# Optimization experiments

Measured on AMD Instinct MI355X. Metric: run time of the kernel, lower is better.

The kernel has to match this reference:

```python
import jax, jax.numpy as jnp
from jax import lax
import numpy as np

LRELU_SLOPE = 0.01  # PyTorch LeakyReLU default
BETA = 0.25


def lrelu(x):
    return jnp.where(x >= 0, x, LRELU_SLOPE * x)


def conv2d(x, w, b, stride, pad):
    # x: [B,C,H,W], w: [Cout,Cin,k,k] (torch OIHW)
    y = lax.conv_general_dilated(x, w, (stride, stride), ((pad, pad), (pad, pad)),
                                 dimension_numbers=('NCHW', 'OIHW', 'NCHW'))
    return y + b[None, :, None, None]


def conv_transpose2d(x, w, b, stride, out_pad):
    # w: torch ConvTranspose2d weight [Cin,Cout,k,k]; implement as dilated conv
    # with spatially flipped kernel. out = (i-1)*stride + k + out_pad.
    wf = jnp.flip(w, (2, 3)).transpose(1, 0, 2, 3)  # -> [Cout,Cin,k,k]
    k = w.shape[2]
    pad = ((k - 1, k - 1 + out_pad), (k - 1, k - 1 + out_pad))
    y = lax.conv_general_dilated(x, wf, (1, 1), pad, lhs_dilation=(stride, stride),
                                 dimension_numbers=('NCHW', 'OIHW', 'NCHW'))
    return y + b[None, :, None, None]


def setup_inputs() -> dict:
    key = jax.random.key(0)
    ks = jax.random.split(key, 16)
    s = 0.05
    inp = {
        'x':   jax.random.normal(ks[0], (64, 1, 256, 256), jnp.float32),
        'ew1': jax.random.normal(ks[1], (8, 1, 4, 4), jnp.float32) * s,
        'eb1': jnp.zeros((8,), jnp.float32),
        'ew2': jax.random.normal(ks[2], (16, 8, 4, 4), jnp.float32) * s,
        'eb2': jnp.zeros((16,), jnp.float32),
        'ew3': jax.random.normal(ks[3], (32, 16, 4, 4), jnp.float32) * s,
        'eb3': jnp.zeros((32,), jnp.float32),
        'ew4': jax.random.normal(ks[4], (32, 32, 3, 3), jnp.float32) * s,
        'eb4': jnp.zeros((32,), jnp.float32),
        'ew5': jax.random.normal(ks[5], (64, 32, 1, 1), jnp.float32) * s,
        'eb5': jnp.zeros((64,), jnp.float32),
        'dw1': jax.random.normal(ks[6], (32, 64, 3, 3), jnp.float32) * s,
        'db1': jnp.zeros((32,), jnp.float32),
        'dw2': jax.random.normal(ks[7], (32, 16, 4, 4), jnp.float32) * s,
        'db2': jnp.zeros((16,), jnp.float32),
        'dw3': jax.random.normal(ks[8], (16, 8, 4, 4), jnp.float32) * s,
        'db3': jnp.zeros((8,), jnp.float32),
        'dw4': jax.random.normal(ks[9], (8, 1, 4, 4), jnp.float32) * s,
        'db4': jnp.zeros((1,), jnp.float32),
        # nn.init.uniform_(-1/K, 1/K) with K=512
        'codebook': jax.random.uniform(ks[10], (512, 64), jnp.float32,
                                       minval=-1.0 / 512, maxval=1.0 / 512),
    }
    return inp


def vqvae_forward(x, ew1, eb1, ew2, eb2, ew3, eb3, ew4, eb4, ew5, eb5,
                  dw1, db1, dw2, db2, dw3, db3, dw4, db4, codebook):
    # ---- encoder ----
    h = lrelu(conv2d(x, ew1, eb1, 2, 0))   # [B,8,127,127]
    h = lrelu(conv2d(h, ew2, eb2, 2, 0))   # [B,16,62,62]
    h = lrelu(conv2d(h, ew3, eb3, 2, 0))   # [B,32,30,30]
    h = lrelu(conv2d(h, ew4, eb4, 1, 1))   # [B,32,30,30]
    h = lrelu(conv2d(h, ew5, eb5, 1, 0))   # [B,64,30,30]
    # ---- vector quantizer ----
    lat = h.transpose(0, 2, 3, 1)                      # [B,h,w,D]
    D = lat.shape[-1]
    flat = lat.reshape(-1, D)                          # [N,D]
    # squared euclidean distances via expansion (same argmin as torch.norm)
    d2 = (jnp.sum(flat * flat, axis=1, keepdims=True)
          - 2.0 * flat @ codebook.T
          + jnp.sum(codebook * codebook, axis=1))      # [N,K]
    idx = jnp.argmin(d2, axis=1)                       # [N]
    q = codebook[idx].reshape(lat.shape)               # [B,h,w,D]
    commitment = jnp.mean((lax.stop_gradient(q) - lat) ** 2)
    embedding = jnp.mean((q - lax.stop_gradient(lat)) ** 2)
    vq_loss = commitment * BETA + embedding
    q_st = lat + lax.stop_gradient(q - lat)            # straight-through
    z = q_st.transpose(0, 3, 1, 2)                     # [B,D,h,w]
    # ---- decoder ----
    h = lrelu(conv2d(z, dw1, db1, 1, 1))               # [B,32,30,30]
    h = lrelu(conv_transpose2d(h, dw2, db2, 2, 1))     # [B,16,63,63]
    h = lrelu(conv_transpose2d(h, dw3, db3, 2, 1))     # [B,8,131,131]
    recons = jnp.tanh(conv_transpose2d(h, dw4, db4, 2, 0))  # [B,1,264,264]
    return recons, vq_loss


def reference(x, ew1, eb1, ew2, eb2, ew3, eb3, ew4, eb4, ew5, eb5,
              dw1, db1, dw2, db2, dw3, db3, dw4, db4, codebook):
    return vqvae_forward(x, ew1, eb1, ew2, eb2, ew3, eb3, ew4, eb4, ew5, eb5,
                         dw1, db1, dw2, db2, dw3, db3, dw4, db4, codebook)
```

## Files before the change

### kernel.cpp

```cpp
#include <hip/hip_runtime.h>
#include <hip/hip_bf16.h>
#include <math.h>

#define LRELU 0.01f

template<int NW>
__device__ __forceinline__ void ldw(const float* p, float* w) {
    if constexpr (NW % 4 == 0) {
#pragma unroll
        for (int u = 0; u < NW / 4; u++) {
            float4 v = *(const float4*)(p + 4 * u);
            w[4*u] = v.x; w[4*u+1] = v.y; w[4*u+2] = v.z; w[4*u+3] = v.w;
        }
    } else {
#pragma unroll
        for (int c = 0; c < NW; c++) w[c] = p[c];
    }
}

__device__ __forceinline__ void wfwd(const float* s, float* d, int CIN, int COUT,
                                     int KK, int i) {
    int co = i / (CIN * KK); int r = i - co * CIN * KK;
    int ci = r / KK; int t = r - ci * KK;
    d[(ci * KK + t) * COUT + co] = s[i];
}
__device__ __forceinline__ void wtr(const float* s, float* d, int CIN, int COUT,
                                    int KK, int i) {
    int ci = i / (COUT * KK); int r = i - ci * COUT * KK;
    int co = r / KK; int t = r - co * KK;
    d[(t * CIN + ci) * COUT + co] = s[i];
}
__global__ __launch_bounds__(256)
void prep_k(const float* e1, const float* e2, const float* e3, const float* e4,
            const float* e5, const float* d1, const float* d2, const float* d3,
            const float* d4, float* w, const float* cbp, float* hcbn,
            unsigned long long* keys, float* loss, int* idxm, int N) {
    int i = blockIdx.x * 256 + threadIdx.x;
    if      (i < 128)   wfwd(e1, w + 0,     1,  8, 16, i);
    else if (i < 2176)  wfwd(e2, w + 128,   8, 16, 16, i - 128);
    else if (i < 10368) wfwd(e3, w + 2176, 16, 32, 16, i - 2176);
    else if (i < 19584) wfwd(e4, w + 10368, 32, 32, 9, i - 10368);
    else if (i < 21632) wfwd(e5, w + 19584, 32, 64, 1, i - 19584);
    else if (i < 40064) wfwd(d1, w + 21632, 64, 32, 9, i - 21632);
    else if (i < 48256) wtr (d2, w + 40064, 32, 16, 16, i - 40064);
    else if (i < 50304) wtr (d3, w + 48256, 16,  8, 16, i - 48256);
    else if (i < 50432) wtr (d4, w + 50304,  8,  1, 16, i - 50304);
    else if (i < 50944) {
        int k = i - 50432;
        const float* c = cbp + k * 64;
        float s = 0.f;
#pragma unroll
        for (int d = 0; d < 64; d++) s = fmaf(c[d], c[d], s);
        hcbn[k] = 0.5f * s;
    } else if (i < 50944 + N) {
        keys[i - 50944] = 0xFFFFFFFFFFFFFFFFull;
    } else if (i == 50944 + N) {
        loss[0] = 0.f;
    } else if (i < 50945 + N + 64 * 124) {
        int j = i - (50945 + N);
        int b2 = j / 124, s = j - b2 * 124;
        int r, c;
        if (s < 32)      { r = 0;  c = s; }
        else if (s < 64) { r = 31; c = s - 32; }
        else { int u = s - 64; r = 1 + (u >> 1); c = (u & 1) * 31; }
        idxm[b2 * 1024 + r * 32 + c] = 512;
    }
}

__global__ __launch_bounds__(256)
void ubuild_k(const float* __restrict__ w, const float* __restrict__ cb,
              float* __restrict__ U) {
    int g = blockIdx.x * 256 + threadIdx.x;
    if (g >= 513 * 288) return;
    if (g >= 512 * 288) { U[g] = 0.f; return; }
    int k = g / 288, rem = g - k * 288;
    const float* cr = cb + k * 64;
    float s = 0.f;
#pragma unroll 4
    for (int ci = 0; ci < 64; ci++)
        s = fmaf(w[ci * 288 + rem], cr[ci], s);
    U[g] = s;
}

template<int CIN, int COUT, int CO_BLK, int HIN, int ISTR, int HOUT, int WOUT,
         int OPLANE, int OSTR, int OPAD, int CB, int RB, int ZCONV, int ZF_CH>
__global__ __launch_bounds__(256)
void convs2_k(const float* __restrict__ in, const float* __restrict__ wt,
              const float* __restrict__ bias, float* __restrict__ out) {
    const int b = blockIdx.x, cog = blockIdx.y, tid = threadIdx.x;
    if (ZF_CH > 0 && (int)blockIdx.z >= ZCONV) {
        if (cog != 0) return;
        int i = ((int)blockIdx.z - ZCONV) * 256 + tid;
        if (i >= ZF_CH * 124) return;
        int ch = i / 124, s = i - ch * 124;
        int r, c;
        if (s < 32)      { r = 0;  c = s; }
        else if (s < 64) { r = 31; c = s - 32; }
        else { int u = s - 64; r = 1 + (u >> 1); c = (u & 1) * 31; }
        out[(size_t)(b * ZF_CH + ch) * 1024 + r * 32 + c] = 0.f;
        return;
    }
    __shared__ __align__(16) float lw[CIN * 16 * CO_BLK];
    for (int i = tid; i < CIN * 16 * CO_BLK; i += 256) {
        int row = i / CO_BLK, c = i - row * CO_BLK;
        lw[i] = wt[row * COUT + cog * CO_BLK + c];
    }
    __syncthreads();

    const int tz = blockIdx.z;
    const int cbi = tz / RB, rb = tz - cbi * RB;
    const int tx = tid & 15, ty = tid >> 4;
    const int ow0 = (cbi * 16 + tx) * 2;
    const int oh  = rb * 16 + ty;
    if (oh >= HOUT || ow0 >= WOUT) return;
    const bool p1v = (ow0 + 1) < WOUT;

    float acc[CO_BLK][2];
#pragma unroll
    for (int c = 0; c < CO_BLK; c++) {
        float bv = bias[cog * CO_BLK + c];
        acc[c][0] = bv; acc[c][1] = bv;
    }
    const float* inb = in + ((size_t)(b * CIN) * HIN + oh * 2) * ISTR + ow0 * 2;
#pragma unroll 2
    for (int ci = 0; ci < CIN; ci++) {
        const float* r = inb + (size_t)ci * HIN * ISTR;
        float4 a4[4]; float2 b2[4];
#pragma unroll
        for (int kh = 0; kh < 4; kh++) {
            a4[kh] = *(const float4*)(r + kh * ISTR);
            b2[kh] = p1v ? *(const float2*)(r + kh * ISTR + 4) : make_float2(0.f, 0.f);
        }
        const float* wr = lw + ci * 16 * CO_BLK;
#pragma unroll
        for (int kh = 0; kh < 4; kh++) {
            float x0[4] = {a4[kh].x, a4[kh].y, a4[kh].z, a4[kh].w};
            float x1[4] = {a4[kh].z, a4[kh].w, b2[kh].x, b2[kh].y};
#pragma unroll
            for (int kw = 0; kw < 4; kw++) {
                float wv[CO_BLK];
                ldw<CO_BLK>(wr + (kh * 4 + kw) * CO_BLK, wv);
#pragma unroll
                for (int c = 0; c < CO_BLK; c++) {
                    acc[c][0] = fmaf(x0[kw], wv[c], acc[c][0]);
                    acc[c][1] = fmaf(x1[kw], wv[c], acc[c][1]);
                }
            }
        }
    }
    float* ob = out + (size_t)(b * COUT + cog * CO_BLK) * OPLANE
                    + (oh + OPAD) * OSTR + ow0 + OPAD;
#pragma unroll
    for (int c = 0; c < CO_BLK; c++) {
        float v0 = acc[c][0]; v0 = (v0 >= 0.f) ? v0 : LRELU * v0;
        ob[(size_t)c * OPLANE] = v0;
        if (p1v) {
            float v1 = acc[c][1]; v1 = (v1 >= 0.f) ? v1 : LRELU * v1;
            ob[(size_t)c * OPLANE + 1] = v1;
        }
    }
}

template<int CIN, int COUT, int CO_BLK, int OPLANE, int OSTR, int OPADH, int OPADV,
         bool ZSIDE>
__global__ __launch_bounds__(256)
void conv3_k(const float* __restrict__ in, const float* __restrict__ wt,
             const float* __restrict__ bias, float* __restrict__ out) {
    const int b = blockIdx.x, cog = blockIdx.y, tid = threadIdx.x;
    __shared__ __align__(16) float lw[CIN * 9 * CO_BLK];
    for (int i = tid; i < CIN * 9 * CO_BLK; i += 256) {
        int row = i / CO_BLK, c = i - row * CO_BLK;
        lw[i] = wt[row * COUT + cog * CO_BLK + c];
    }
    __syncthreads();

    const int rb = blockIdx.z;
    const int tx = tid & 15, ty = tid >> 4;
    const int r = rb * 16 + ty;
    if (r >= 30) return;
    const int ow0 = tx * 2;
    if (tx == 15) {
        if (ZSIDE) {
#pragma unroll
            for (int c = 0; c < CO_BLK; c++) {
                float* base = out + (size_t)(b * COUT + cog * CO_BLK + c) * OPLANE
                                  + (r + OPADV) * OSTR;
                base[0] = 0.f; base[31] = 0.f; base[32] = 0.f;
            }
        }
        return;
    }
    float acc[CO_BLK][2];
#pragma unroll
    for (int c = 0; c < CO_BLK; c++) {
        float bv = bias[cog * CO_BLK + c];
        acc[c][0] = bv; acc[c][1] = bv;
    }
    const float* inb = in + ((size_t)(b * CIN) * 32 + r) * 32 + ow0;
#pragma unroll 2
    for (int ci = 0; ci < CIN; ci++) {
        const float* rr = inb + (size_t)ci * 1024;
        float2 A[3], Bv[3];
#pragma unroll
        for (int kh = 0; kh < 3; kh++) {
            A[kh]  = *(const float2*)(rr + kh * 32);
            Bv[kh] = *(const float2*)(rr + kh * 32 + 2);
        }
        const float* wr = lw + ci * 9 * CO_BLK;
#pragma unroll
        for (int kh = 0; kh < 3; kh++) {
            float x0[3] = {A[kh].x, A[kh].y, Bv[kh].x};
            float x1[3] = {A[kh].y, Bv[kh].x, Bv[kh].y};
#pragma unroll
            for (int kw = 0; kw < 3; kw++) {
                float wv[CO_BLK];
                ldw<CO_BLK>(wr + (kh * 3 + kw) * CO_BLK, wv);
#pragma unroll
                for (int c = 0; c < CO_BLK; c++) {
                    acc[c][0] = fmaf(x0[kw], wv[c], acc[c][0]);
                    acc[c][1] = fmaf(x1[kw], wv[c], acc[c][1]);
                }
            }
        }
    }
    float* ob = out + (size_t)(b * COUT + cog * CO_BLK) * OPLANE
                    + (r + OPADV) * OSTR + ow0 + OPADH;
#pragma unroll
    for (int c = 0; c < CO_BLK; c++) {
        float v0 = acc[c][0]; v0 = (v0 >= 0.f) ? v0 : LRELU * v0;
        float v1 = acc[c][1]; v1 = (v1 >= 0.f) ? v1 : LRELU * v1;
        ob[(size_t)c * OPLANE] = v0;
        ob[(size_t)c * OPLANE + 1] = v1;
    }
}

template<int CIN, int COUT, int CO_BLK>
__global__ __launch_bounds__(256)
void conv1_k(const float* __restrict__ in, const float* __restrict__ wt,
             const float* __restrict__ bias, float* __restrict__ out) {
    __shared__ __align__(16) float lw[CIN * CO_BLK];
    const int b = blockIdx.x, cog = blockIdx.y;
    for (int i = threadIdx.x; i < CIN * CO_BLK; i += 256) {
        int row = i / CO_BLK, c = i - row * CO_BLK;
        lw[i] = wt[row * COUT + cog * CO_BLK + c];
    }
    __syncthreads();

    const int px4 = threadIdx.x * 4;
    float acc[CO_BLK][4];
#pragma unroll
    for (int c = 0; c < CO_BLK; c++) {
        float bv = bias[cog * CO_BLK + c];
        acc[c][0] = bv; acc[c][1] = bv; acc[c][2] = bv; acc[c][3] = bv;
    }
#pragma unroll 4
    for (int ci = 0; ci < CIN; ci++) {
        float4 x = *(const float4*)(in + (size_t)(b * CIN + ci) * 1024 + px4);
        float wv[CO_BLK];
        ldw<CO_BLK>(lw + ci * CO_BLK, wv);
#pragma unroll
        for (int c = 0; c < CO_BLK; c++) {
            acc[c][0] = fmaf(x.x, wv[c], acc[c][0]);
            acc[c][1] = fmaf(x.y, wv[c], acc[c][1]);
            acc[c][2] = fmaf(x.z, wv[c], acc[c][2]);
            acc[c][3] = fmaf(x.w, wv[c], acc[c][3]);
        }
    }
#pragma unroll
    for (int c = 0; c < CO_BLK; c++) {
        float4 v;
        v.x = (acc[c][0] >= 0.f) ? acc[c][0] : LRELU * acc[c][0];
        v.y = (acc[c][1] >= 0.f) ? acc[c][1] : LRELU * acc[c][1];
        v.z = (acc[c][2] >= 0.f) ? acc[c][2] : LRELU * acc[c][2];
        v.w = (acc[c][3] >= 0.f) ? acc[c][3] : LRELU * acc[c][3];
        *(float4*)(out + (size_t)(b * COUT + cog * CO_BLK + c) * 1024 + px4) = v;
    }
}

__global__ __launch_bounds__(256)
void d1tab_k(const int* __restrict__ idxm, const float* __restrict__ U,
             const float* __restrict__ bias, float* __restrict__ out) {
    const int b = blockIdx.x, cog = blockIdx.y, rt = blockIdx.z;
    const int tx = threadIdx.x & 31, ty = threadIdx.x >> 5;
    const int r = rt * 8 + ty;
    if (r >= 30) return;
    if (tx >= 30) {
        if (tx == 31) {
#pragma unroll
            for (int c = 0; c < 16; c++) {
                float* base = out + (size_t)(b * 32 + cog * 16 + c) * 1020 + r * 34;
                base[1] = 0.f; base[32] = 0.f; base[33] = 0.f;
            }
        }
        return;
    }
    const int* im = idxm + b * 1024 + r * 32 + tx;
    float acc[16];
#pragma unroll
    for (int c = 0; c < 16; c++) acc[c] = bias[cog * 16 + c];
#pragma unroll
    for (int kh = 0; kh < 3; kh++) {
        int i0 = im[kh * 32 + 0];
        int i1 = im[kh * 32 + 1];
        int i2 = im[kh * 32 + 2];
        const float4* u0 = (const float4*)(U + ((size_t)i0 * 9 + kh * 3 + 0) * 32 + cog * 16);
        const float4* u1 = (const float4*)(U + ((size_t)i1 * 9 + kh * 3 + 1) * 32 + cog * 16);
        const float4* u2 = (const float4*)(U + ((size_t)i2 * 9 + kh * 3 + 2) * 32 + cog * 16);
#pragma unroll
        for (int q = 0; q < 4; q++) {
            float4 a = u0[q], bb = u1[q], cc = u2[q];
            acc[4*q+0] += (a.x + bb.x) + cc.x;
            acc[4*q+1] += (a.y + bb.y) + cc.y;
            acc[4*q+2] += (a.z + bb.z) + cc.z;
            acc[4*q+3] += (a.w + bb.w) + cc.w;
        }
    }
    float* ob = out + (size_t)(b * 32 + cog * 16) * 1020 + r * 34 + tx + 2;
#pragma unroll
    for (int c = 0; c < 16; c++) {
        float v = acc[c]; v = (v >= 0.f) ? v : LRELU * v;
        ob[(size_t)c * 1020] = v;
    }
}

template<int CIN, int COUT, int CO_BLK, int HIN, int ISTR, int HOUT, int WOUT,
         int OPLANE, int OSTR, int OPADH, int NTX, int NT,
         int ZS_CH, int ZS_H, int ZS_STR, int ZC0, int ZC1, int ZC2,
         bool DO_TANH, bool DO_LOSS>
__global__ __launch_bounds__(256)
void convtf_k(const float* __restrict__ in, const float* __restrict__ wt,
              const float* __restrict__ bias, float* __restrict__ out,
              const float* __restrict__ loss, float* __restrict__ losstgt) {
    const int b = blockIdx.x, tid = threadIdx.x;
    const int NCOG = COUT / CO_BLK;
    int zz = blockIdx.z;
    if (zz >= NCOG * NT) {
        if (DO_LOSS) {
            if (b == 0 && tid == 0)
                losstgt[0] = 1.25f * loss[0] / (57600.f * 64.f);
            return;
        }
        int i = (zz - NCOG * NT) * 256 + tid;
        if (i >= ZS_CH * ZS_H * 3) return;
        int ch = i / (ZS_H * 3); int u = i - ch * ZS_H * 3;
        int r = u / 3, c3 = u - r * 3;
        int col = (c3 == 0) ? ZC0 : (c3 == 1) ? ZC1 : ZC2;
        out[((size_t)(b * ZS_CH + ch) * ZS_H + r) * ZS_STR + col] = 0.f;
        return;
    }
    const int cog = zz / NT, tile = zz - cog * NT;
    const int tlx = tile % NTX, tly = tile / NTX;

    __shared__ __align__(16) float lw[16 * CIN * CO_BLK];
    for (int i = tid; i < 16 * CIN * CO_BLK; i += 256) {
        int aq = i / (CIN * 4 * CO_BLK);
        int r1 = i - aq * (CIN * 4 * CO_BLK);
        int ci = r1 / (4 * CO_BLK);
        int u  = r1 - ci * (4 * CO_BLK);
        int pp = u / CO_BLK, c = u - pp * CO_BLK;
        int a = aq >> 1, q = aq & 1, py = pp >> 1, px = pp & 1;
        int tap = (py + 2 * a) * 4 + px + 2 * q;
        lw[i] = wt[((size_t)tap * CIN + ci) * COUT + cog * CO_BLK + c];
    }
    __syncthreads();

    const int SX = (WOUT + 1) >> 1, SY = (HOUT + 1) >> 1;
    const int sx0 = tlx * 32 + (tid & 15);
    const int sx1 = sx0 + 16;
    const int sy  = tly * 16 + (tid >> 4);
    const bool v0 = sx0 < SX, v1 = sx1 < SX;
    if (sy >= SY || !(v0 || v1)) return;

    const bool rvA = (sy < HIN);
    const bool rvB = (sy >= 1) && (sy <= HIN);

    float acc[2][4][CO_BLK];
#pragma unroll
    for (int s = 0; s < 2; s++)
#pragma unroll
        for (int o = 0; o < 4; o++)
#pragma unroll
            for (int c = 0; c < CO_BLK; c++)
                acc[s][o][c] = bias[cog * CO_BLK + c];

    const float* base = in + (size_t)(b * CIN) * HIN * ISTR;
#pragma unroll 2
    for (int ci = 0; ci < CIN; ci++) {
        const float* rowA = base + (size_t)ci * HIN * ISTR + (size_t)sy * ISTR;
        const float* rowB = rowA - ISTR;
        float rA0x = 0.f, rA0y = 0.f, rA1x = 0.f, rA1y = 0.f;
        float rB0x = 0.f, rB0y = 0.f, rB1x = 0.f, rB1y = 0.f;
        if (rvA) {
            if (v0) { rA0x = rowA[sx0]; rA0y = rowA[sx0 + 1]; }
            if (v1) { rA1x = rowA[sx1]; rA1y = rowA[sx1 + 1]; }
        }
        if (rvB) {
            if (v0) { rB0x = rowB[sx0]; rB0y = rowB[sx0 + 1]; }
            if (v1) { rB1x = rowB[sx1]; rB1y = rowB[sx1 + 1]; }
        }
#pragma unroll
        for (int a = 0; a < 2; a++) {
#pragma unroll
            for (int q = 0; q < 2; q++) {
                float iv0 = q ? (a ? rB0x : rA0x) : (a ? rB0y : rA0y);
                float iv1 = q ? (a ? rB1x : rA1x) : (a ? rB1y : rA1y);
                const float* wp = lw + (size_t)((a * 2 + q) * CIN + ci) * (4 * CO_BLK);
                float wv[4 * CO_BLK];
                ldw<4 * CO_BLK>(wp, wv);
#pragma unroll
                for (int o = 0; o < 4; o++)
#pragma unroll
                    for (int c = 0; c < CO_BLK; c++) {
                        acc[0][o][c] = fmaf(iv0, wv[o * CO_BLK + c], acc[0][o][c]);
                        acc[1][o][c] = fmaf(iv1, wv[o * CO_BLK + c], acc[1][o][c]);
                    }
            }
        }
    }
#pragma unroll
    for (int s = 0; s < 2; s++) {
        if (s ? !v1 : !v0) continue;
        const int sxx = s ? sx1 : sx0;
        const int ow = 2 * sxx;
        const bool full = (ow + 1) < WOUT;
#pragma unroll
        for (int py = 0; py < 2; py++) {
            int oh = 2 * sy + py;
            if (oh >= HOUT) continue;
            float* ob = out + (size_t)(b * COUT + cog * CO_BLK) * OPLANE
                            + (size_t)oh * OSTR + ow + OPADH;
#pragma unroll
            for (int c = 0; c < CO_BLK; c++) {
                float va = acc[s][py * 2 + 0][c];
                float vb = acc[s][py * 2 + 1][c];
                if (DO_TANH) { va = tanhf(va); vb = tanhf(vb); }
                else {
                    va = (va >= 0.f) ? va : LRELU * va;
                    vb = (vb >= 0.f) ? vb : LRELU * vb;
                }
                if ((OPADH & 1) == 0 && full) {
                    *(float2*)(ob + (size_t)c * OPLANE) = make_float2(va, vb);
                } else {
                    ob[(size_t)c * OPLANE] = va;
                    if (full) ob[(size_t)c * OPLANE + 1] = vb;
                }
            }
        }
    }
}

__global__ __launch_bounds__(256, 4)
void vq_argmin_k(const float* __restrict__ lat, const float* __restrict__ cb,
                 const float* __restrict__ hcbn,
                 unsigned long long* __restrict__ keys) {
    const int pb = blockIdx.x;
    if (pb >= 225) return;
    const int pos = pb * 256 + threadIdx.x;
    const int kbase = blockIdx.y * 64;

    int b = pos / 900, p = pos - b * 900;
    int oh = p / 30, ow = p - oh * 30;
    int pp = 33 + oh * 32 + ow;
    const float* lb = lat + (size_t)b * 64 * 1024 + pp;
    float l[64];
#pragma unroll
    for (int d = 0; d < 64; d++) l[d] = lb[(size_t)d * 1024];
    asm volatile("" ::: "memory");

    float best = 3.4e38f;
    int   bi   = 0;
#pragma unroll 1
    for (int k = 0; k < 64; k++) {
        const float4* cp = (const float4*)(cb + (size_t)(kbase + k) * 64);
        float hn = hcbn[kbase + k];
        float4 c[16];
#pragma unroll
        for (int u = 0; u < 16; u++) c[u] = cp[u];
        float a0 = 0.f, a1 = 0.f, a2 = 0.f, a3 = 0.f;
#pragma unroll
        for (int u = 0; u < 16; u++) {
            a0 = fmaf(l[4*u+0], c[u].x, a0);
            a1 = fmaf(l[4*u+1], c[u].y, a1);
            a2 = fmaf(l[4*u+2], c[u].z, a2);
            a3 = fmaf(l[4*u+3], c[u].w, a3);
        }
        float score = hn - ((a0 + a1) + (a2 + a3));
        if (score < best) { best = score; bi = kbase + k; }
    }
    unsigned u = __float_as_uint(best);
    u = ((int)u < 0) ? ~u : (u | 0x80000000u);
    unsigned long long key = ((unsigned long long)u << 32) | (unsigned)bi;
    atomicMin(&keys[pos], key);
}

__global__ __launch_bounds__(256)
void vq_finalize_k(const float* __restrict__ lat, const float* __restrict__ cb,
                   const unsigned long long* __restrict__ keys,
                   int* __restrict__ idxm, float* __restrict__ loss_acc, int B) {
    int gid = blockIdx.x * 256 + threadIdx.x;
    const int N = B * 900;
    float myloss = 0.f;
    if (gid < N) {
        int b = gid / 900, p = gid - b * 900;
        int oh = p / 30, ow = p - oh * 30;
        int pp = 33 + oh * 32 + ow;
        int idx = (int)(unsigned)(keys[gid] & 0xFFFFFFFFull);
        idxm[b * 1024 + pp] = idx;
        const float4* crow = (const float4*)(cb + (size_t)idx * 64);
        const float* lrow = lat + (size_t)b * 64 * 1024 + pp;
#pragma unroll
        for (int i = 0; i < 16; i++) {
            float4 cv = crow[i];
            float lv0 = lrow[(4 * i + 0) * 1024];
            float lv1 = lrow[(4 * i + 1) * 1024];
            float lv2 = lrow[(4 * i + 2) * 1024];
            float lv3 = lrow[(4 * i + 3) * 1024];
            float d0 = cv.x - lv0, d1 = cv.y - lv1, d2 = cv.z - lv2, d3 = cv.w - lv3;
            myloss = fmaf(d0, d0, myloss);
            myloss = fmaf(d1, d1, myloss);
            myloss = fmaf(d2, d2, myloss);
            myloss = fmaf(d3, d3, myloss);
        }
    }
    __shared__ float red[256];
    red[threadIdx.x] = myloss;
    __syncthreads();
    for (int s = 128; s > 0; s >>= 1) {
        if ((int)threadIdx.x < s) red[threadIdx.x] += red[threadIdx.x + s];
        __syncthreads();
    }
    if (threadIdx.x == 0) atomicAdd(loss_acc, red[0]);
}

static inline int nblk(long long total) { return (int)((total + 255) / 256); }

extern "C" void kernel_launch(void* const* d_in, const int* in_sizes, int n_in,
                              void* d_out, int out_size, void* d_ws, size_t ws_size,
                              hipStream_t stream) {
    const float* x   = (const float*)d_in[0];
    const float* ew1 = (const float*)d_in[1];  const float* eb1 = (const float*)d_in[2];
    const float* ew2 = (const float*)d_in[3];  const float* eb2 = (const float*)d_in[4];
    const float* ew3 = (const float*)d_in[5];  const float* eb3 = (const float*)d_in[6];
    const float* ew4 = (const float*)d_in[7];  const float* eb4 = (const float*)d_in[8];
    const float* ew5 = (const float*)d_in[9];  const float* eb5 = (const float*)d_in[10];
    const float* dw1 = (const float*)d_in[11]; const float* db1 = (const float*)d_in[12];
    const float* dw2 = (const float*)d_in[13]; const float* db2 = (const float*)d_in[14];
    const float* dw3 = (const float*)d_in[15]; const float* db3 = (const float*)d_in[16];
    const float* dw4 = (const float*)d_in[17]; const float* db4 = (const float*)d_in[18];
    const float* cb  = (const float*)d_in[19];
    float* out = (float*)d_out;

    const int B = in_sizes[0] / (256 * 256);
    const int N = B * 900;

    char* ws = (char*)d_ws;
    float* A     = (float*)(ws);
    float* Bb    = (float*)(ws + 34873344);
    float* d2out = (float*)(ws + 34873344);
    float* d3out = (float*)(ws);
    unsigned long long* keys = (unsigned long long*)(ws + 51126272);
    float* hcbn  = (float*)(ws + 51587072);
    int*   idxm  = (int*)(ws + 51589120);
    float* loss  = (float*)(ws + 52420608);
    float* wtb   = (float*)(ws + 52420864);
    float* U     = (float*)(ws + 52622592);
    float* ew1t = wtb;          float* ew2t = wtb + 128;
    float* ew3t = wtb + 2176;   float* ew4t = wtb + 10368;
    float* ew5t = wtb + 19584;  float* dw1t = wtb + 21632;
    float* dw2t = wtb + 40064;  float* dw3t = wtb + 48256;
    float* dw4t = wtb + 50304;

    prep_k<<<nblk(50945 + N + 64 * 124), 256, 0, stream>>>(
        ew1, ew2, ew3, ew4, ew5, dw1, dw2, dw3, dw4, wtb,
        cb, hcbn, keys, loss, idxm, N);
    ubuild_k<<<nblk(513 * 288), 256, 0, stream>>>(dw1t, cb, U);

    convs2_k<1, 8, 8, 256, 256, 127, 127, 127 * 128, 128, 0, 4, 8, 32, 0>
        <<<dim3(B, 1, 32), 256, 0, stream>>>(x, ew1t, eb1, A);
    convs2_k<8, 16, 4, 127, 128, 62, 62, 62 * 64, 64, 0, 2, 4, 8, 0>
        <<<dim3(B, 4, 8), 256, 0, stream>>>(A, ew2t, eb2, Bb);
    convs2_k<16, 32, 4, 62, 64, 30, 30, 1024, 32, 1, 1, 2, 2, 32>
        <<<dim3(B, 8, 18), 256, 0, stream>>>(Bb, ew3t, eb3, A);
    conv3_k<32, 32, 4, 1024, 32, 1, 1, false>
        <<<dim3(B, 8, 2), 256, 0, stream>>>(A, ew4t, eb4, Bb);
    conv1_k<32, 64, 4><<<dim3(B, 16, 1), 256, 0, stream>>>(Bb, ew5t, eb5, A);

    vq_argmin_k<<<dim3(232, 8), 256, 0, stream>>>(A, cb, hcbn, keys);
    vq_finalize_k<<<nblk(N), 256, 0, stream>>>(A, cb, keys, idxm, loss, B);

    d1tab_k<<<dim3(B, 2, 4), 256, 0, stream>>>(idxm, U, db1, A);
    convtf_k<32, 16, 4, 30, 34, 63, 63, 63 * 68, 68, 2, 1, 2,
             16, 63, 68, 1, 65, 66, false, false>
        <<<dim3(B, 1, 20), 256, 0, stream>>>(A + 1, dw2t, db2, d2out,
                                             nullptr, nullptr);
    convtf_k<16, 8, 8, 63, 68, 129, 129, 129 * 132, 132, 2, 3, 15,
             8, 129, 132, 1, 1, 131, false, false>
        <<<dim3(B, 1, 28), 256, 0, stream>>>(d2out + 1, dw3t, db3, d3out,
                                             nullptr, nullptr);
    convtf_k<8, 1, 1, 129, 132, 260, 260, 67600, 260, 0, 5, 45,
             0, 1, 1, 0, 0, 0, true, true>
        <<<dim3(B, 1, 46), 256, 0, stream>>>(d3out + 1, dw4t, db4, out, loss,
                                             out + (out_size - 1));
}
```

Baseline: 407.3 us.

## Write latent in compact NHWC layout for contiguous VQ loads

The 1x1 conv now writes the latent as a compact [pos][64] NHWC buffer, dropping the padded border, rather than as padded NCHW planes. The VQ argmin and finalize kernels then read each position's 64-dim vector with float4 loads instead of 64 strided scalar loads. The argmin inner loop also loads codebook rows inside the FMA loop instead of staging them in a register array. The conv's stores become 16-byte scattered writes with a border test, and it assumes the A buffer can hold the compact layout.

```diff
diff --git a/kernel.cpp b/kernel.cpp
--- a/kernel.cpp
+++ b/kernel.cpp
@@ -234,32 +234,31 @@
     }
 }
 
-template<int CIN, int COUT, int CO_BLK>
-__global__ __launch_bounds__(256)
-void conv1_k(const float* __restrict__ in, const float* __restrict__ wt,
-             const float* __restrict__ bias, float* __restrict__ out) {
-    __shared__ __align__(16) float lw[CIN * CO_BLK];
+__global__ __launch_bounds__(256)
+void conv1nhwc_k(const float* __restrict__ in, const float* __restrict__ wt,
+                 const float* __restrict__ bias, float* __restrict__ latf) {
+    __shared__ __align__(16) float lw[32 * 4];
     const int b = blockIdx.x, cog = blockIdx.y;
-    for (int i = threadIdx.x; i < CIN * CO_BLK; i += 256) {
-        int row = i / CO_BLK, c = i - row * CO_BLK;
-        lw[i] = wt[row * COUT + cog * CO_BLK + c];
+    for (int i = threadIdx.x; i < 32 * 4; i += 256) {
+        int row = i / 4, c = i - row * 4;
+        lw[i] = wt[row * 64 + cog * 4 + c];
     }
     __syncthreads();
 
     const int px4 = threadIdx.x * 4;
-    float acc[CO_BLK][4];
-#pragma unroll
-    for (int c = 0; c < CO_BLK; c++) {
-        float bv = bias[cog * CO_BLK + c];
+    float acc[4][4];
+#pragma unroll
+    for (int c = 0; c < 4; c++) {
+        float bv = bias[cog * 4 + c];
         acc[c][0] = bv; acc[c][1] = bv; acc[c][2] = bv; acc[c][3] = bv;
     }
 #pragma unroll 4
-    for (int ci = 0; ci < CIN; ci++) {
-        float4 x = *(const float4*)(in + (size_t)(b * CIN + ci) * 1024 + px4);
-        float wv[CO_BLK];
-        ldw<CO_BLK>(lw + ci * CO_BLK, wv);
-#pragma unroll
-        for (int c = 0; c < CO_BLK; c++) {
+    for (int ci = 0; ci < 32; ci++) {
+        float4 x = *(const float4*)(in + (size_t)(b * 32 + ci) * 1024 + px4);
+        float wv[4];
+        ldw<4>(lw + ci * 4, wv);
+#pragma unroll
+        for (int c = 0; c < 4; c++) {
             acc[c][0] = fmaf(x.x, wv[c], acc[c][0]);
             acc[c][1] = fmaf(x.y, wv[c], acc[c][1]);
             acc[c][2] = fmaf(x.z, wv[c], acc[c][2]);
@@ -267,13 +266,18 @@
         }
     }
 #pragma unroll
-    for (int c = 0; c < CO_BLK; c++) {
-        float4 v;
-        v.x = (acc[c][0] >= 0.f) ? acc[c][0] : LRELU * acc[c][0];
-        v.y = (acc[c][1] >= 0.f) ? acc[c][1] : LRELU * acc[c][1];
-        v.z = (acc[c][2] >= 0.f) ? acc[c][2] : LRELU * acc[c][2];
-        v.w = (acc[c][3] >= 0.f) ? acc[c][3] : LRELU * acc[c][3];
-        *(float4*)(out + (size_t)(b * COUT + cog * CO_BLK + c) * 1024 + px4) = v;
+    for (int j = 0; j < 4; j++) {
+        int pix = px4 + j;
+        int row = pix >> 5, col = pix & 31;
+        if (row >= 1 && row <= 30 && col >= 1 && col <= 30) {
+            int pos = b * 900 + (row - 1) * 30 + (col - 1);
+            float4 v;
+            v.x = (acc[0][j] >= 0.f) ? acc[0][j] : LRELU * acc[0][j];
+            v.y = (acc[1][j] >= 0.f) ? acc[1][j] : LRELU * acc[1][j];
+            v.z = (acc[2][j] >= 0.f) ? acc[2][j] : LRELU * acc[2][j];
+            v.w = (acc[3][j] >= 0.f) ? acc[3][j] : LRELU * acc[3][j];
+            *(float4*)(latf + (size_t)pos * 64 + cog * 4) = v;
+        }
     }
 }
 
@@ -450,7 +454,7 @@
 }
 
 __global__ __launch_bounds__(256, 4)
-void vq_argmin_k(const float* __restrict__ lat, const float* __restrict__ cb,
+void vq_argmin_k(const float* __restrict__ latf, const float* __restrict__ cb,
                  const float* __restrict__ hcbn,
                  unsigned long long* __restrict__ keys) {
     const int pb = blockIdx.x;
@@ -458,14 +462,10 @@
     const int pos = pb * 256 + threadIdx.x;
     const int kbase = blockIdx.y * 64;
 
-    int b = pos / 900, p = pos - b * 900;
-    int oh = p / 30, ow = p - oh * 30;
-    int pp = 33 + oh * 32 + ow;
-    const float* lb = lat + (size_t)b * 64 * 1024 + pp;
-    float l[64];
-#pragma unroll
-    for (int d = 0; d < 64; d++) l[d] = lb[(size_t)d * 1024];
-    asm volatile("" ::: "memory");
+    const float4* lp = (const float4*)(latf + (size_t)pos * 64);
+    float4 L[16];
+#pragma unroll
+    for (int i = 0; i < 16; i++) L[i] = lp[i];
 
     float best = 3.4e38f;
     int   bi   = 0;
@@ -473,16 +473,14 @@
     for (int k = 0; k < 64; k++) {
         const float4* cp = (const float4*)(cb + (size_t)(kbase + k) * 64);
         float hn = hcbn[kbase + k];
-        float4 c[16];
-#pragma unroll
-        for (int u = 0; u < 16; u++) c[u] = cp[u];
         float a0 = 0.f, a1 = 0.f, a2 = 0.f, a3 = 0.f;
 #pragma unroll
         for (int u = 0; u < 16; u++) {
-            a0 = fmaf(l[4*u+0], c[u].x, a0);
-            a1 = fmaf(l[4*u+1], c[u].y, a1);
-            a2 = fmaf(l[4*u+2], c[u].z, a2);
-            a3 = fmaf(l[4*u+3], c[u].w, a3);
+            float4 c = cp[u];
+            a0 = fmaf(L[u].x, c.x, a0);
+            a1 = fmaf(L[u].y, c.y, a1);
+            a2 = fmaf(L[u].z, c.z, a2);
+            a3 = fmaf(L[u].w, c.w, a3);
         }
         float score = hn - ((a0 + a1) + (a2 + a3));
         if (score < best) { best = score; bi = kbase + k; }
@@ -494,7 +492,7 @@
 }
 
 __global__ __launch_bounds__(256)
-void vq_finalize_k(const float* __restrict__ lat, const float* __restrict__ cb,
+void vq_finalize_k(const float* __restrict__ latf, const float* __restrict__ cb,
                    const unsigned long long* __restrict__ keys,
                    int* __restrict__ idxm, float* __restrict__ loss_acc, int B) {
     int gid = blockIdx.x * 256 + threadIdx.x;
@@ -507,15 +505,13 @@
         int idx = (int)(unsigned)(keys[gid] & 0xFFFFFFFFull);
         idxm[b * 1024 + pp] = idx;
         const float4* crow = (const float4*)(cb + (size_t)idx * 64);
-        const float* lrow = lat + (size_t)b * 64 * 1024 + pp;
+        const float4* lrow = (const float4*)(latf + (size_t)gid * 64);
 #pragma unroll
         for (int i = 0; i < 16; i++) {
             float4 cv = crow[i];
-            float lv0 = lrow[(4 * i + 0) * 1024];
-            float lv1 = lrow[(4 * i + 1) * 1024];
-            float lv2 = lrow[(4 * i + 2) * 1024];
-            float lv3 = lrow[(4 * i + 3) * 1024];
-            float d0 = cv.x - lv0, d1 = cv.y - lv1, d2 = cv.z - lv2, d3 = cv.w - lv3;
+            float4 lv = lrow[i];
+            float d0 = cv.x - lv.x, d1 = cv.y - lv.y;
+            float d2 = cv.z - lv.z, d3 = cv.w - lv.w;
             myloss = fmaf(d0, d0, myloss);
             myloss = fmaf(d1, d1, myloss);
             myloss = fmaf(d2, d2, myloss);
@@ -583,7 +579,7 @@
         <<<dim3(B, 8, 18), 256, 0, stream>>>(Bb, ew3t, eb3, A);
     conv3_k<32, 32, 4, 1024, 32, 1, 1, false>
         <<<dim3(B, 8, 2), 256, 0, stream>>>(A, ew4t, eb4, Bb);
-    conv1_k<32, 64, 4><<<dim3(B, 16, 1), 256, 0, stream>>>(Bb, ew5t, eb5, A);
+    conv1nhwc_k<<<dim3(B, 16, 1), 256, 0, stream>>>(Bb, ew5t, eb5, A);
 
     vq_argmin_k<<<dim3(232, 8), 256, 0, stream>>>(A, cb, hcbn, keys);
     vq_finalize_k<<<nblk(N), 256, 0, stream>>>(A, cb, keys, idxm, loss, B);
```

After: 414.1 us. Within noise of the previous version (+1.7%).
